# Kernel optimization log

Measured on AMD Instinct MI355X. Metric: run time of the kernel, lower is better.

Reference implementation:

```python
import jax, jax.numpy as jnp
import numpy as np

N_NODES = 20000
N_EDGES = 320000
D_IN = 128
D_OUT = 128
HEADS = 12
BN_EPS = 1e-5


def setup_inputs() -> dict:
    key = jax.random.key(0)
    ks = jax.random.split(key, 24)
    x = jax.random.normal(ks[0], (N_NODES, D_IN), dtype=jnp.float32)
    # edges guaranteed to have no self loops (so remove_self_loops is a no-op)
    src = jax.random.randint(ks[1], (N_EDGES,), 0, N_NODES, dtype=jnp.int32)
    off = jax.random.randint(ks[2], (N_EDGES,), 1, N_NODES, dtype=jnp.int32)
    dst = (src + off) % N_NODES
    edge_index = jnp.stack([src, dst], axis=0)
    inp = {"x": x, "edge_index": edge_index}
    # per-layer FeatureSteeredConvolution params (torch init: uniform weights, N(0,0.1) c/bias)
    dims_in = [D_IN, D_OUT, D_OUT]
    k = 3
    for li in range(3):
        din = dims_in[li]
        inp[f"l{li}_Wlin"] = jax.random.uniform(ks[k], (HEADS * D_OUT, din), dtype=jnp.float32); k += 1
        inp[f"l{li}_Wu"] = jax.random.uniform(ks[k], (HEADS, din), dtype=jnp.float32); k += 1
        inp[f"l{li}_c"] = 0.1 * jax.random.normal(ks[k], (HEADS,), dtype=jnp.float32); k += 1
        inp[f"l{li}_b"] = 0.1 * jax.random.normal(ks[k], (D_OUT,), dtype=jnp.float32); k += 1
    for bi in range(2):
        inp[f"bn{bi}_g"] = jnp.ones((D_OUT,), dtype=jnp.float32)
        inp[f"bn{bi}_b"] = jnp.zeros((D_OUT,), dtype=jnp.float32)
    return inp


def _fsc(x, src, dst, Wlin, Wu, c, b):
    """FeatureSteeredConvolution: edge gather -> softmax attention over heads ->
    per-head linear -> scatter-mean over destination nodes."""
    n = x.shape[0]
    x_j = x[src]                                  # [E, Cin] source features
    x_i = x[dst]                                  # [E, Cin] target features
    att = jax.nn.softmax((x_i - x_j) @ Wu.T + c, axis=1)   # [E, H]
    Wl = Wlin.reshape(HEADS, D_OUT, -1)           # [H, Cout, Cin]
    msg = jnp.zeros((src.shape[0], D_OUT), dtype=x.dtype)
    for h in range(HEADS):                        # small fixed loop over heads
        msg = msg + att[:, h:h + 1] * (x_j @ Wl[h].T)
    agg = jax.ops.segment_sum(msg, dst, num_segments=n)
    deg = jax.ops.segment_sum(jnp.ones((dst.shape[0],), dtype=x.dtype), dst, num_segments=n)
    return agg / jnp.maximum(deg, 1.0)[:, None] + b


def _bn(x, g, b):
    # BatchNorm1d in training mode: biased batch statistics
    m = jnp.mean(x, axis=0)
    v = jnp.var(x, axis=0)
    return (x - m) * jax.lax.rsqrt(v + BN_EPS) * g + b


def reference(x, edge_index, l0_Wlin, l0_Wu, l0_c, l0_b, bn0_g, bn0_b,
              l1_Wlin, l1_Wu, l1_c, l1_b, bn1_g, bn1_b,
              l2_Wlin, l2_Wu, l2_c, l2_b):
    n = x.shape[0]
    loops = jnp.arange(n, dtype=edge_index.dtype)
    src = jnp.concatenate([edge_index[0], loops])
    dst = jnp.concatenate([edge_index[1], loops])
    h = jax.nn.relu(_fsc(x, src, dst, l0_Wlin, l0_Wu, l0_c, l0_b))
    h = _bn(h, bn0_g, bn0_b)
    h = jax.nn.relu(_fsc(h, src, dst, l1_Wlin, l1_Wu, l1_c, l1_b))
    h = _bn(h, bn1_g, bn1_b)
    return _fsc(h, src, dst, l2_Wlin, l2_Wu, l2_c, l2_b)
```

## Files before the change

kernel.cpp:

```cpp
#include <hip/hip_runtime.h>
#include <hip/hip_bf16.h>

#define DHID 128
#define NH 12
#define KDIM 1536
#define KSPLIT 3
#define KS (KDIM / KSPLIT)
#define NSTATB 128

typedef __attribute__((ext_vector_type(8))) short short8;
typedef __attribute__((ext_vector_type(4))) float f32x4;

static __device__ __forceinline__ unsigned short f2bf(float f) {
  __hip_bfloat16 h = __float2bfloat16(f);
  return __builtin_bit_cast(unsigned short, h);
}


__global__ void hist_k(const int* __restrict__ dstp, int* __restrict__ cnt, int e0, int et) {
  int e = blockIdx.x * blockDim.x + threadIdx.x;
  if (e >= et) return;
  int d = (e < e0) ? dstp[e] : (e - e0);
  atomicAdd(&cnt[d], 1);
}

__global__ void scan_k(const int* __restrict__ cnt, int* __restrict__ row_start,
                       int* __restrict__ cursor, int n, int total) {
  __shared__ int part[1024];
  int t = threadIdx.x;
  const int CH = (n + 1023) >> 10;
  int base = t * CH;
  int s = 0;
  for (int j = 0; j < CH; ++j) { int i = base + j; if (i < n) s += cnt[i]; }
  part[t] = s;
  __syncthreads();
  for (int off = 1; off < 1024; off <<= 1) {
    int v = (t >= off) ? part[t - off] : 0;
    __syncthreads();
    part[t] += v;
    __syncthreads();
  }
  int run = (t == 0) ? 0 : part[t - 1];
  for (int j = 0; j < CH; ++j) {
    int i = base + j;
    if (i < n) {
      int c = cnt[i];
      row_start[i] = run;
      cursor[i] = run;
      run += c;
    }
  }
  if (t == 0) row_start[n] = total;
}

__global__ void scatter_k(const int* __restrict__ srcp, const int* __restrict__ dstp,
                          int* __restrict__ cursor, int* __restrict__ srcs,
                          int* __restrict__ dsts, int e0, int et) {
  int e = blockIdx.x * blockDim.x + threadIdx.x;
  if (e >= et) return;
  int s = (e < e0) ? srcp[e] : (e - e0);
  int d = (e < e0) ? dstp[e] : (e - e0);
  int pos = atomicAdd(&cursor[d], 1);
  srcs[pos] = s;
  dsts[pos] = d;
}


__global__ void u_k(const float* __restrict__ x, const float* __restrict__ Wu,
                    float* __restrict__ u, int n) {
  int wid = (blockIdx.x * blockDim.x + threadIdx.x) >> 6;
  if (wid >= n) return;
  int lane = threadIdx.x & 63;
  float2 xv = *(const float2*)(x + (long)wid * DHID + 2 * lane);
  #pragma unroll
  for (int h = 0; h < NH; ++h) {
    float2 wv = *(const float2*)(Wu + h * DHID + 2 * lane);
    float p = xv.x * wv.x + xv.y * wv.y;
    p += __shfl_xor(p, 1);  p += __shfl_xor(p, 2);  p += __shfl_xor(p, 4);
    p += __shfl_xor(p, 8);  p += __shfl_xor(p, 16); p += __shfl_xor(p, 32);
    if (lane == 0) u[wid * NH + h] = p;
  }
}


__global__ void att_k(const float* __restrict__ u, const float* __restrict__ cvec,
                      const int* __restrict__ srcs, const int* __restrict__ dsts,
                      const int* __restrict__ row_start, float* __restrict__ attS, int et) {
  int j = blockIdx.x * blockDim.x + threadIdx.x;
  if (j >= et) return;
  int s = srcs[j], d = dsts[j];
  const float4* ud = (const float4*)(u + (long)d * NH);
  const float4* us = (const float4*)(u + (long)s * NH);
  const float4* cp = (const float4*)cvec;
  float w[NH];
  #pragma unroll
  for (int q = 0; q < 3; ++q) {
    float4 a = ud[q], b = us[q], c = cp[q];
    w[4*q+0] = a.x - b.x + c.x;
    w[4*q+1] = a.y - b.y + c.y;
    w[4*q+2] = a.z - b.z + c.z;
    w[4*q+3] = a.w - b.w + c.w;
  }
  float m = w[0];
  #pragma unroll
  for (int h = 1; h < NH; ++h) m = fmaxf(m, w[h]);
  float ssum = 0.f;
  #pragma unroll
  for (int h = 0; h < NH; ++h) { w[h] = __expf(w[h] - m); ssum += w[h]; }
  float deg = (float)(row_start[d + 1] - row_start[d]);
  float inv = 1.f / (ssum * deg);
  float4* op = (float4*)(attS + (long)j * NH);
  #pragma unroll
  for (int q = 0; q < 3; ++q) {
    float4 v;
    v.x = w[4*q+0] * inv; v.y = w[4*q+1] * inv;
    v.z = w[4*q+2] * inv; v.w = w[4*q+3] * inv;
    op[q] = v;
  }
}


__global__ void edge_k(const float* __restrict__ x, const float* __restrict__ attS,
                       const int* __restrict__ srcs, const int* __restrict__ row_start,
                       unsigned short* __restrict__ A, int n) {
  int wid = __builtin_amdgcn_readfirstlane((int)((blockIdx.x * blockDim.x + threadIdx.x) >> 6));
  if (wid >= n) return;
  int lane = threadIdx.x & 63;
  float acc[NH][2];
  #pragma unroll
  for (int h = 0; h < NH; ++h) { acc[h][0] = 0.f; acc[h][1] = 0.f; }
  int beg = row_start[wid], end = row_start[wid + 1];
  int j = beg;
  for (; j + 3 < end; j += 4) {
    int sx[4];
    #pragma unroll
    for (int i = 0; i < 4; ++i) sx[i] = srcs[j + i];
    float2 xv[4];
    #pragma unroll
    for (int i = 0; i < 4; ++i)
      xv[i] = *(const float2*)(x + (long)sx[i] * DHID + 2 * lane);
    const float4* ap = (const float4*)(attS + (long)j * NH);
    float4 aq[4][3];
    #pragma unroll
    for (int i = 0; i < 4; ++i) {
      aq[i][0] = ap[i * 3 + 0];
      aq[i][1] = ap[i * 3 + 1];
      aq[i][2] = ap[i * 3 + 2];
    }
    #pragma unroll
    for (int i = 0; i < 4; ++i) {
      float av[NH];
      av[0]=aq[i][0].x; av[1]=aq[i][0].y; av[2] =aq[i][0].z; av[3] =aq[i][0].w;
      av[4]=aq[i][1].x; av[5]=aq[i][1].y; av[6] =aq[i][1].z; av[7] =aq[i][1].w;
      av[8]=aq[i][2].x; av[9]=aq[i][2].y; av[10]=aq[i][2].z; av[11]=aq[i][2].w;
      #pragma unroll
      for (int h = 0; h < NH; ++h) {
        acc[h][0] += av[h] * xv[i].x;
        acc[h][1] += av[h] * xv[i].y;
      }
    }
  }
  for (; j < end; ++j) {
    int s0 = srcs[j];
    float2 xv0 = *(const float2*)(x + (long)s0 * DHID + 2 * lane);
    const float4* a0p = (const float4*)(attS + (long)j * NH);
    float4 a00 = a0p[0], a01 = a0p[1], a02 = a0p[2];
    float av0[NH];
    av0[0]=a00.x; av0[1]=a00.y; av0[2]=a00.z;  av0[3]=a00.w;
    av0[4]=a01.x; av0[5]=a01.y; av0[6]=a01.z;  av0[7]=a01.w;
    av0[8]=a02.x; av0[9]=a02.y; av0[10]=a02.z; av0[11]=a02.w;
    #pragma unroll
    for (int h = 0; h < NH; ++h) {
      acc[h][0] += av0[h] * xv0.x;
      acc[h][1] += av0[h] * xv0.y;
    }
  }
  unsigned* Ap = (unsigned*)(A + (long)wid * KDIM);
  #pragma unroll
  for (int h = 0; h < NH; ++h) {
    unsigned pv = (unsigned)f2bf(acc[h][0]) | ((unsigned)f2bf(acc[h][1]) << 16);
    Ap[h * (DHID / 2) + lane] = pv;
  }
}


__global__ void prep_wcat_k(const float* __restrict__ Wlin, unsigned short* __restrict__ Wcat) {
  int t = blockIdx.x * blockDim.x + threadIdx.x;
  int c = t / KDIM, f = t - c * KDIM;
  int h = f >> 7, k = f & (DHID - 1);
  Wcat[t] = f2bf(Wlin[((h << 7) + c) * DHID + k]);
}


__global__ __launch_bounds__(256) void gemm_k(
    const unsigned short* __restrict__ A, const unsigned short* __restrict__ B,
    float* __restrict__ part, float* __restrict__ outp, int M) {
  int w = threadIdx.x >> 6, lane = threadIdx.x & 63;
  int lr = lane & 15, lq = lane >> 4;
  int m0 = blockIdx.x * 64, n0 = w * 32;
  int ks = blockIdx.y;
  if (m0 >= M) return;
  f32x4 acc[4][2];
  #pragma unroll
  for (int mf = 0; mf < 4; ++mf)
    #pragma unroll
    for (int nf = 0; nf < 2; ++nf) acc[mf][nf] = (f32x4){0.f, 0.f, 0.f, 0.f};
  const short* Ap = (const short*)A;
  const short* Bp = (const short*)B;
  long arow[4], brow[2];
  #pragma unroll
  for (int mf = 0; mf < 4; ++mf) arow[mf] = (long)(m0 + mf * 16 + lr) * KDIM + lq * 8;
  #pragma unroll
  for (int nf = 0; nf < 2; ++nf) brow[nf] = (long)(n0 + nf * 16 + lr) * KDIM + lq * 8;
  const int kbeg = ks * KS, kend = kbeg + KS;
  #pragma unroll 2
  for (int kk = kbeg; kk < kend; kk += 32) {
    short8 av[4], bv[2];
    #pragma unroll
    for (int mf = 0; mf < 4; ++mf) av[mf] = *(const short8*)(Ap + arow[mf] + kk);
    #pragma unroll
    for (int nf = 0; nf < 2; ++nf) bv[nf] = *(const short8*)(Bp + brow[nf] + kk);
    #pragma unroll
    for (int mf = 0; mf < 4; ++mf)
      #pragma unroll
      for (int nf = 0; nf < 2; ++nf)
        acc[mf][nf] = __builtin_amdgcn_mfma_f32_16x16x32_bf16(av[mf], bv[nf], acc[mf][nf], 0, 0, 0);
  }
  float* op = (ks == 0) ? outp : (part + (long)(ks - 1) * M * DHID);
  #pragma unroll
  for (int mf = 0; mf < 4; ++mf) {
    #pragma unroll
    for (int nf = 0; nf < 2; ++nf) {
      int c = n0 + nf * 16 + lr;
      int rowb = m0 + mf * 16 + lq * 4;
      #pragma unroll
      for (int r = 0; r < 4; ++r) {
        int row = rowb + r;
        if (row < M) op[(long)row * DHID + c] = acc[mf][nf][r];
      }
    }
  }
}


__global__ void combine_k(const float* __restrict__ part, const float* __restrict__ bias,
                          float* __restrict__ outp, int M, int relu) {
  int t = blockIdx.x * blockDim.x + threadIdx.x;
  int nvec = M * (DHID / 4);
  if (t >= nvec) return;
  long idx = (long)t * 4;
  int c = (t & 31) * 4;
  float4 p0 = *(const float4*)(outp + idx);
  float4 p1 = *(const float4*)(part + idx);
  float4 p2 = *(const float4*)(part + (long)M * DHID + idx);
  float4 bc = *(const float4*)(bias + c);
  float4 v;
  v.x = p0.x + p1.x + p2.x + bc.x;
  v.y = p0.y + p1.y + p2.y + bc.y;
  v.z = p0.z + p1.z + p2.z + bc.z;
  v.w = p0.w + p1.w + p2.w + bc.w;
  if (relu) {
    v.x = fmaxf(v.x, 0.f); v.y = fmaxf(v.y, 0.f);
    v.z = fmaxf(v.z, 0.f); v.w = fmaxf(v.w, 0.f);
  }
  *(float4*)(outp + idx) = v;
}


__global__ __launch_bounds__(256) void bnstat_k(const float* __restrict__ buf,
                                                float* __restrict__ bnpart, int nvec) {
  int t = blockIdx.x * 256 + threadIdx.x;
  const int stride = NSTATB * 256;
  float s0=0,s1=0,s2=0,s3=0,q0=0,q1=0,q2=0,q3=0;
  for (int i = t; i < nvec; i += stride) {
    float4 v = *(const float4*)(buf + (long)i * 4);
    s0 += v.x; s1 += v.y; s2 += v.z; s3 += v.w;
    q0 += v.x*v.x; q1 += v.y*v.y; q2 += v.z*v.z; q3 += v.w*v.w;
  }
  s0 += __shfl_xor(s0, 32); s1 += __shfl_xor(s1, 32);
  s2 += __shfl_xor(s2, 32); s3 += __shfl_xor(s3, 32);
  q0 += __shfl_xor(q0, 32); q1 += __shfl_xor(q1, 32);
  q2 += __shfl_xor(q2, 32); q3 += __shfl_xor(q3, 32);
  __shared__ float red[4][256];
  int w = threadIdx.x >> 6, lane = threadIdx.x & 63;
  if (lane < 32) {
    int cb = lane * 4;
    red[w][cb+0] = s0; red[w][cb+1] = s1; red[w][cb+2] = s2; red[w][cb+3] = s3;
    red[w][128+cb+0] = q0; red[w][128+cb+1] = q1; red[w][128+cb+2] = q2; red[w][128+cb+3] = q3;
  }
  __syncthreads();
  int tt = threadIdx.x;
  float p = red[0][tt] + red[1][tt] + red[2][tt] + red[3][tt];
  bnpart[blockIdx.x * 256 + tt] = p;
}


__global__ void bnfin_k(const float* __restrict__ bnpart,
                        const float* __restrict__ g, const float* __restrict__ b,
                        float* __restrict__ sc, float* __restrict__ sh, float invn) {
  __shared__ float col[256];
  int t = threadIdx.x;
  float s = 0.f;
  #pragma unroll 8
  for (int bb = 0; bb < NSTATB; ++bb) s += bnpart[bb * 256 + t];
  col[t] = s;
  __syncthreads();
  if (t < DHID) {
    float m = col[t] * invn;
    float v = col[128 + t] * invn - m * m;
    float rs = rsqrtf(v + 1e-5f);
    float sg = g[t] * rs;
    sc[t] = sg;
    sh[t] = b[t] - m * sg;
  }
}

__global__ void bnapply_k(float* __restrict__ buf, const float* __restrict__ sc,
                          const float* __restrict__ sh, int nvec) {
  int i = blockIdx.x * blockDim.x + threadIdx.x;
  if (i >= nvec) return;
  long idx = (long)i * 4;
  int c = (int)(idx & (DHID - 1));
  float4 v = *(const float4*)(buf + idx);
  v.x = v.x * sc[c]     + sh[c];
  v.y = v.y * sc[c + 1] + sh[c + 1];
  v.z = v.z * sc[c + 2] + sh[c + 2];
  v.w = v.w * sc[c + 3] + sh[c + 3];
  *(float4*)(buf + idx) = v;
}


extern "C" void kernel_launch(void* const* d_in, const int* in_sizes, int n_in,
                              void* d_out, int out_size, void* d_ws, size_t ws_size,
                              hipStream_t stream) {
  const float* x = (const float*)d_in[0];
  const int* ei = (const int*)d_in[1];
  const int N = in_sizes[0] / DHID;
  const int E0 = in_sizes[1] / 2;
  const int ET = E0 + N;
  const int* srcp = ei;
  const int* dstp = ei + E0;
  const float* Wlin[3] = {(const float*)d_in[2], (const float*)d_in[6], (const float*)d_in[10]};
  const float* Wu[3]   = {(const float*)d_in[3], (const float*)d_in[7], (const float*)d_in[11]};
  const float* cc[3]   = {(const float*)d_in[4], (const float*)d_in[8], (const float*)d_in[12]};
  const float* bb[3]   = {(const float*)d_in[5], (const float*)d_in[9], (const float*)d_in[13]};
  const float* bng[2]  = {(const float*)d_in[14], (const float*)d_in[16]};
  const float* bnb[2]  = {(const float*)d_in[15], (const float*)d_in[17]};

  const int MPAD = ((N + 63) / 64) * 64;

  size_t o = 0;
  char* base = (char*)d_ws;
  auto carve = [&](size_t bytes) -> char* {
    char* p = base + o;
    o += (bytes + 255) & ~(size_t)255;
    return p;
  };
  int* row_start = (int*)carve((size_t)(N + 1) * 4);
  int* cursor    = (int*)carve((size_t)N * 4);
  int* srcs      = (int*)carve((size_t)ET * 4);
  int* dsts      = (int*)carve((size_t)ET * 4);
  float* u       = (float*)carve((size_t)N * NH * 4);
  float* bnpart  = (float*)carve((size_t)NSTATB * 256 * 4);
  float* bnsc    = (float*)carve((size_t)DHID * 4);
  float* bnsh    = (float*)carve((size_t)DHID * 4);
  unsigned short* Wcat = (unsigned short*)carve((size_t)DHID * KDIM * 2);
  size_t attS_bytes = (size_t)ET * NH * 4;
  size_t part_bytes = (size_t)(KSPLIT - 1) * N * DHID * 4;
  char* shared_rg = carve(attS_bytes > part_bytes ? attS_bytes : part_bytes);
  float* attS = (float*)shared_rg;
  float* partb = (float*)shared_rg;
  float* hA      = (float*)carve((size_t)N * DHID * 4);
  unsigned short* A = (unsigned short*)carve((size_t)MPAD * KDIM * 2);
  (void)ws_size; (void)n_in; (void)out_size;

  const int EB = (ET + 255) / 256;
  const int NW = (N + 3) / 4;
  const int MB64 = (N + 63) / 64;
  const int AV = (N * DHID / 4 + 255) / 256;

  hipMemsetAsync(cursor, 0, (size_t)N * 4, stream);
  hist_k<<<EB, 256, 0, stream>>>(dstp, cursor, E0, ET);
  scan_k<<<1, 1024, 0, stream>>>(cursor, row_start, cursor, N, ET);
  scatter_k<<<EB, 256, 0, stream>>>(srcp, dstp, cursor, srcs, dsts, E0, ET);

  const float* hin = x;
  for (int li = 0; li < 3; ++li) {
    const bool last = (li == 2);
    u_k<<<NW, 256, 0, stream>>>(hin, Wu[li], u, N);
    att_k<<<EB, 256, 0, stream>>>(u, cc[li], srcs, dsts, row_start, attS, ET);
    edge_k<<<NW, 256, 0, stream>>>(hin, attS, srcs, row_start, A, N);
    prep_wcat_k<<<(DHID * KDIM) / 256, 256, 0, stream>>>(Wlin[li], Wcat);
    float* outp = last ? (float*)d_out : hA;
    gemm_k<<<dim3(MB64, KSPLIT), 256, 0, stream>>>(A, Wcat, partb, outp, N);
    combine_k<<<AV, 256, 0, stream>>>(partb, bb[li], outp, N, last ? 0 : 1);
    if (!last) {
      bnstat_k<<<NSTATB, 256, 0, stream>>>(hA, bnpart, N * DHID / 4);
      bnfin_k<<<1, 256, 0, stream>>>(bnpart, bng[li], bnb[li], bnsc, bnsh, 1.f / (float)N);
      bnapply_k<<<AV, 256, 0, stream>>>(hA, bnsc, bnsh, N * DHID / 4);
      hin = hA;
    }
  }
}
```

Measured before the change: 543.1 us.

## Gather node features in bf16 and use a four-way GEMM K-split when workspace allows

Converts the input features, and each later batch-normalised hidden layer, into a bf16 copy. The attention-logit and edge-aggregation kernels then read half as many bytes per gathered neighbour row. The GEMM is templated on the K-slice length, picks a 4-way split when the workspace is large enough, and unrolls its loop more deeply. This trades a small precision loss in the gathered features for less gather bandwidth, at the cost of an extra conversion kernel and more partial-sum traffic in the combine step.

```diff
diff --git a/kernel.cpp b/kernel.cpp
--- a/kernel.cpp
+++ b/kernel.cpp
@@ -4,8 +4,6 @@
 #define DHID 128
 #define NH 12
 #define KDIM 1536
-#define KSPLIT 3
-#define KS (KDIM / KSPLIT)
 #define NSTATB 128
 
 typedef __attribute__((ext_vector_type(8))) short short8;
@@ -14,6 +12,10 @@
 static __device__ __forceinline__ unsigned short f2bf(float f) {
   __hip_bfloat16 h = __float2bfloat16(f);
   return __builtin_bit_cast(unsigned short, h);
+}
+static __device__ __forceinline__ float bf2f(unsigned short u) {
+  unsigned v = ((unsigned)u) << 16;
+  return __builtin_bit_cast(float, v);
 }
 
 
@@ -66,16 +68,29 @@
 }
 
 
-__global__ void u_k(const float* __restrict__ x, const float* __restrict__ Wu,
+__global__ void cvt_k(const float* __restrict__ in, unsigned short* __restrict__ outp, int nvec) {
+  int t = blockIdx.x * blockDim.x + threadIdx.x;
+  if (t >= nvec) return;
+  long idx = (long)t * 4;
+  float4 v = *(const float4*)(in + idx);
+  uint2 r;
+  r.x = (unsigned)f2bf(v.x) | ((unsigned)f2bf(v.y) << 16);
+  r.y = (unsigned)f2bf(v.z) | ((unsigned)f2bf(v.w) << 16);
+  *(uint2*)(outp + idx) = r;
+}
+
+
+__global__ void u_k(const unsigned short* __restrict__ xb, const float* __restrict__ Wu,
                     float* __restrict__ u, int n) {
   int wid = (blockIdx.x * blockDim.x + threadIdx.x) >> 6;
   if (wid >= n) return;
   int lane = threadIdx.x & 63;
-  float2 xv = *(const float2*)(x + (long)wid * DHID + 2 * lane);
+  unsigned pv = *(const unsigned*)(xb + (long)wid * DHID + 2 * lane);
+  float x0 = bf2f((unsigned short)pv), x1 = bf2f((unsigned short)(pv >> 16));
   #pragma unroll
   for (int h = 0; h < NH; ++h) {
     float2 wv = *(const float2*)(Wu + h * DHID + 2 * lane);
-    float p = xv.x * wv.x + xv.y * wv.y;
+    float p = x0 * wv.x + x1 * wv.y;
     p += __shfl_xor(p, 1);  p += __shfl_xor(p, 2);  p += __shfl_xor(p, 4);
     p += __shfl_xor(p, 8);  p += __shfl_xor(p, 16); p += __shfl_xor(p, 32);
     if (lane == 0) u[wid * NH + h] = p;
@@ -120,7 +135,7 @@
 }
 
 
-__global__ void edge_k(const float* __restrict__ x, const float* __restrict__ attS,
+__global__ void edge_k(const unsigned short* __restrict__ xb, const float* __restrict__ attS,
                        const int* __restrict__ srcs, const int* __restrict__ row_start,
                        unsigned short* __restrict__ A, int n) {
   int wid = __builtin_amdgcn_readfirstlane((int)((blockIdx.x * blockDim.x + threadIdx.x) >> 6));
@@ -135,10 +150,10 @@
     int sx[4];
     #pragma unroll
     for (int i = 0; i < 4; ++i) sx[i] = srcs[j + i];
-    float2 xv[4];
+    unsigned pv[4];
     #pragma unroll
     for (int i = 0; i < 4; ++i)
-      xv[i] = *(const float2*)(x + (long)sx[i] * DHID + 2 * lane);
+      pv[i] = *(const unsigned*)(xb + (long)sx[i] * DHID + 2 * lane);
     const float4* ap = (const float4*)(attS + (long)j * NH);
     float4 aq[4][3];
     #pragma unroll
@@ -149,20 +164,24 @@
     }
     #pragma unroll
     for (int i = 0; i < 4; ++i) {
+      float xv0 = bf2f((unsigned short)pv[i]);
+      float xv1 = bf2f((unsigned short)(pv[i] >> 16));
       float av[NH];
       av[0]=aq[i][0].x; av[1]=aq[i][0].y; av[2] =aq[i][0].z; av[3] =aq[i][0].w;
       av[4]=aq[i][1].x; av[5]=aq[i][1].y; av[6] =aq[i][1].z; av[7] =aq[i][1].w;
       av[8]=aq[i][2].x; av[9]=aq[i][2].y; av[10]=aq[i][2].z; av[11]=aq[i][2].w;
       #pragma unroll
       for (int h = 0; h < NH; ++h) {
-        acc[h][0] += av[h] * xv[i].x;
-        acc[h][1] += av[h] * xv[i].y;
+        acc[h][0] += av[h] * xv0;
+        acc[h][1] += av[h] * xv1;
       }
     }
   }
   for (; j < end; ++j) {
     int s0 = srcs[j];
-    float2 xv0 = *(const float2*)(x + (long)s0 * DHID + 2 * lane);
+    unsigned pv = *(const unsigned*)(xb + (long)s0 * DHID + 2 * lane);
+    float xv0 = bf2f((unsigned short)pv);
+    float xv1 = bf2f((unsigned short)(pv >> 16));
     const float4* a0p = (const float4*)(attS + (long)j * NH);
     float4 a00 = a0p[0], a01 = a0p[1], a02 = a0p[2];
     float av0[NH];
@@ -171,8 +190,8 @@
     av0[8]=a02.x; av0[9]=a02.y; av0[10]=a02.z; av0[11]=a02.w;
     #pragma unroll
     for (int h = 0; h < NH; ++h) {
-      acc[h][0] += av0[h] * xv0.x;
-      acc[h][1] += av0[h] * xv0.y;
+      acc[h][0] += av0[h] * xv0;
+      acc[h][1] += av0[h] * xv1;
     }
   }
   unsigned* Ap = (unsigned*)(A + (long)wid * KDIM);
@@ -192,6 +211,7 @@
 }
 
 
+template<int KSL>
 __global__ __launch_bounds__(256) void gemm_k(
     const unsigned short* __restrict__ A, const unsigned short* __restrict__ B,
     float* __restrict__ part, float* __restrict__ outp, int M) {
@@ -207,14 +227,14 @@
     for (int nf = 0; nf < 2; ++nf) acc[mf][nf] = (f32x4){0.f, 0.f, 0.f, 0.f};
   const short* Ap = (const short*)A;
   const short* Bp = (const short*)B;
+  const long kbeg = (long)ks * KSL;
   long arow[4], brow[2];
   #pragma unroll
-  for (int mf = 0; mf < 4; ++mf) arow[mf] = (long)(m0 + mf * 16 + lr) * KDIM + lq * 8;
-  #pragma unroll
-  for (int nf = 0; nf < 2; ++nf) brow[nf] = (long)(n0 + nf * 16 + lr) * KDIM + lq * 8;
-  const int kbeg = ks * KS, kend = kbeg + KS;
-  #pragma unroll 2
-  for (int kk = kbeg; kk < kend; kk += 32) {
+  for (int mf = 0; mf < 4; ++mf) arow[mf] = (long)(m0 + mf * 16 + lr) * KDIM + lq * 8 + kbeg;
+  #pragma unroll
+  for (int nf = 0; nf < 2; ++nf) brow[nf] = (long)(n0 + nf * 16 + lr) * KDIM + lq * 8 + kbeg;
+  #pragma unroll 4
+  for (int kk = 0; kk < KSL; kk += 32) {
     short8 av[4], bv[2];
     #pragma unroll
     for (int mf = 0; mf < 4; ++mf) av[mf] = *(const short8*)(Ap + arow[mf] + kk);
@@ -243,6 +263,7 @@
 }
 
 
+template<int NP>
 __global__ void combine_k(const float* __restrict__ part, const float* __restrict__ bias,
                           float* __restrict__ outp, int M, int relu) {
   int t = blockIdx.x * blockDim.x + threadIdx.x;
@@ -250,15 +271,14 @@
   if (t >= nvec) return;
   long idx = (long)t * 4;
   int c = (t & 31) * 4;
-  float4 p0 = *(const float4*)(outp + idx);
-  float4 p1 = *(const float4*)(part + idx);
-  float4 p2 = *(const float4*)(part + (long)M * DHID + idx);
+  float4 v = *(const float4*)(outp + idx);
   float4 bc = *(const float4*)(bias + c);
-  float4 v;
-  v.x = p0.x + p1.x + p2.x + bc.x;
-  v.y = p0.y + p1.y + p2.y + bc.y;
-  v.z = p0.z + p1.z + p2.z + bc.z;
-  v.w = p0.w + p1.w + p2.w + bc.w;
+  v.x += bc.x; v.y += bc.y; v.z += bc.z; v.w += bc.w;
+  #pragma unroll
+  for (int p = 0; p < NP; ++p) {
+    float4 pp = *(const float4*)(part + (long)p * M * DHID + idx);
+    v.x += pp.x; v.y += pp.y; v.z += pp.z; v.w += pp.w;
+  }
   if (relu) {
     v.x = fmaxf(v.x, 0.f); v.y = fmaxf(v.y, 0.f);
     v.z = fmaxf(v.z, 0.f); v.w = fmaxf(v.w, 0.f);
@@ -315,8 +335,8 @@
   }
 }
 
-__global__ void bnapply_k(float* __restrict__ buf, const float* __restrict__ sc,
-                          const float* __restrict__ sh, int nvec) {
+__global__ void bnapply_k(float* __restrict__ buf, unsigned short* __restrict__ xb,
+                          const float* __restrict__ sc, const float* __restrict__ sh, int nvec) {
   int i = blockIdx.x * blockDim.x + threadIdx.x;
   if (i >= nvec) return;
   long idx = (long)i * 4;
@@ -327,6 +347,10 @@
   v.z = v.z * sc[c + 2] + sh[c + 2];
   v.w = v.w * sc[c + 3] + sh[c + 3];
   *(float4*)(buf + idx) = v;
+  uint2 r;
+  r.x = (unsigned)f2bf(v.x) | ((unsigned)f2bf(v.y) << 16);
+  r.y = (unsigned)f2bf(v.z) | ((unsigned)f2bf(v.w) << 16);
+  *(uint2*)(xb + idx) = r;
 }
 
 
@@ -349,6 +373,16 @@
 
   const int MPAD = ((N + 63) / 64) * 64;
 
+  auto al = [](size_t b) { return (b + 255) & ~(size_t)255; };
+  const size_t slice = (size_t)N * DHID * 4;
+  const size_t attS_bytes = (size_t)ET * NH * 4;
+  size_t fixed = al((size_t)(N + 1) * 4) + al((size_t)N * 4) + 2 * al((size_t)ET * 4) +
+                 al((size_t)N * NH * 4) + al((size_t)NSTATB * 256 * 4) + 2 * al((size_t)DHID * 4) +
+                 al((size_t)DHID * KDIM * 2) + al(slice) + al((size_t)N * DHID * 2) +
+                 al((size_t)MPAD * KDIM * 2);
+  size_t need4 = fixed + al(attS_bytes > 3 * slice ? attS_bytes : 3 * slice);
+  const int ksplit = (ws_size >= need4) ? 4 : 3;
+
   size_t o = 0;
   char* base = (char*)d_ws;
   auto carve = [&](size_t bytes) -> char* {
@@ -365,14 +399,14 @@
   float* bnsc    = (float*)carve((size_t)DHID * 4);
   float* bnsh    = (float*)carve((size_t)DHID * 4);
   unsigned short* Wcat = (unsigned short*)carve((size_t)DHID * KDIM * 2);
-  size_t attS_bytes = (size_t)ET * NH * 4;
-  size_t part_bytes = (size_t)(KSPLIT - 1) * N * DHID * 4;
+  float* hA      = (float*)carve(slice);
+  unsigned short* xb = (unsigned short*)carve((size_t)N * DHID * 2);
+  unsigned short* A  = (unsigned short*)carve((size_t)MPAD * KDIM * 2);
+  size_t part_bytes = (size_t)(ksplit - 1) * slice;
   char* shared_rg = carve(attS_bytes > part_bytes ? attS_bytes : part_bytes);
   float* attS = (float*)shared_rg;
   float* partb = (float*)shared_rg;
-  float* hA      = (float*)carve((size_t)N * DHID * 4);
-  unsigned short* A = (unsigned short*)carve((size_t)MPAD * KDIM * 2);
-  (void)ws_size; (void)n_in; (void)out_size;
+  (void)n_in; (void)out_size;
 
   const int EB = (ET + 255) / 256;
   const int NW = (N + 3) / 4;
@@ -383,22 +417,26 @@
   hist_k<<<EB, 256, 0, stream>>>(dstp, cursor, E0, ET);
   scan_k<<<1, 1024, 0, stream>>>(cursor, row_start, cursor, N, ET);
   scatter_k<<<EB, 256, 0, stream>>>(srcp, dstp, cursor, srcs, dsts, E0, ET);
-
-  const float* hin = x;
+  cvt_k<<<AV, 256, 0, stream>>>(x, xb, N * DHID / 4);
+
   for (int li = 0; li < 3; ++li) {
     const bool last = (li == 2);
-    u_k<<<NW, 256, 0, stream>>>(hin, Wu[li], u, N);
+    u_k<<<NW, 256, 0, stream>>>(xb, Wu[li], u, N);
     att_k<<<EB, 256, 0, stream>>>(u, cc[li], srcs, dsts, row_start, attS, ET);
-    edge_k<<<NW, 256, 0, stream>>>(hin, attS, srcs, row_start, A, N);
+    edge_k<<<NW, 256, 0, stream>>>(xb, attS, srcs, row_start, A, N);
     prep_wcat_k<<<(DHID * KDIM) / 256, 256, 0, stream>>>(Wlin[li], Wcat);
     float* outp = last ? (float*)d_out : hA;
-    gemm_k<<<dim3(MB64, KSPLIT), 256, 0, stream>>>(A, Wcat, partb, outp, N);
-    combine_k<<<AV, 256, 0, stream>>>(partb, bb[li], outp, N, last ? 0 : 1);
+    if (ksplit == 4) {
+      gemm_k<KDIM / 4><<<dim3(MB64, 4), 256, 0, stream>>>(A, Wcat, partb, outp, N);
+      combine_k<3><<<AV, 256, 0, stream>>>(partb, bb[li], outp, N, last ? 0 : 1);
+    } else {
+      gemm_k<KDIM / 3><<<dim3(MB64, 3), 256, 0, stream>>>(A, Wcat, partb, outp, N);
+      combine_k<2><<<AV, 256, 0, stream>>>(partb, bb[li], outp, N, last ? 0 : 1);
+    }
     if (!last) {
       bnstat_k<<<NSTATB, 256, 0, stream>>>(hA, bnpart, N * DHID / 4);
       bnfin_k<<<1, 256, 0, stream>>>(bnpart, bng[li], bnb[li], bnsc, bnsh, 1.f / (float)N);
-      bnapply_k<<<AV, 256, 0, stream>>>(hA, bnsc, bnsh, N * DHID / 4);
-      hin = hA;
-    }
-  }
-}
+      bnapply_k<<<AV, 256, 0, stream>>>(hA, xb, bnsc, bnsh, N * DHID / 4);
+    }
+  }
+}
```

After: 543.9 us. Within noise of the previous version (+0.1%).
